# Performance work log

Measured on AMD Instinct MI355X. Metric: run time of the kernel, lower is better.

The kernel has to match this reference:

```python
import jax, jax.numpy as jnp
import numpy as np

N_NODES = 50000


def _gcn_conv(x, W, b, src, dst, n_nodes):
    """PyG-style GCNConv: add self-loops, symmetric normalization,
    transform-then-propagate: out = D^-1/2 A_hat D^-1/2 (x W) + b."""
    # add self loops
    loop = jnp.arange(n_nodes, dtype=src.dtype)
    s = jnp.concatenate([src, loop])
    d = jnp.concatenate([dst, loop])
    # degree (edge weight = 1) computed on destination nodes, incl. self loops
    deg = jax.ops.segment_sum(jnp.ones_like(d, dtype=x.dtype), d, num_segments=n_nodes)
    dinv = jnp.where(deg > 0, jax.lax.rsqrt(deg), 0.0)
    norm = dinv[s] * dinv[d]                      # [E+N]
    h = x @ W                                      # [N, F_out]
    msg = h[s] * norm[:, None]                     # [E+N, F_out] gather
    out = jax.ops.segment_sum(msg, d, num_segments=n_nodes)  # scatter-add
    return out + b


def setup_inputs() -> dict:
    key = jax.random.key(0)
    ks = jax.random.split(key, 12)
    N, E = N_NODES, 800000
    input_dim, hidden_dim, latent_dim, output_dim = 256, 64, 32, 3

    def glorot(k, fan_in, fan_out):
        lim = float(np.sqrt(6.0 / (fan_in + fan_out)))
        return jax.random.uniform(k, (fan_in, fan_out), jnp.float32, -lim, lim)

    return {
        "x": jax.random.normal(ks[0], (N, input_dim), jnp.float32),
        "edge_index": jax.random.randint(ks[1], (2, E), 0, N, jnp.int64 if jax.config.jax_enable_x64 else jnp.int32),
        "edge_attr": jax.random.normal(ks[2], (E,), jnp.float32),
        "W_enc_gnn": glorot(ks[3], input_dim, hidden_dim),
        "b_enc_gnn": jnp.zeros((hidden_dim,), jnp.float32),
        "W_enc_fc": glorot(ks[4], hidden_dim, latent_dim),
        "b_enc_fc": jnp.zeros((latent_dim,), jnp.float32),
        "W_dec_fc": glorot(ks[5], latent_dim, hidden_dim),
        "b_dec_fc": jnp.zeros((hidden_dim,), jnp.float32),
        "W_dec_gnn": glorot(ks[6], hidden_dim, input_dim),
        "b_dec_gnn": jnp.zeros((input_dim,), jnp.float32),
        "W_cond": glorot(ks[7], latent_dim, output_dim),
        "b_cond": jnp.zeros((output_dim,), jnp.float32),
    }


def reference(x, edge_index, edge_attr,
              W_enc_gnn, b_enc_gnn, W_enc_fc, b_enc_fc,
              W_dec_fc, b_dec_fc, W_dec_gnn, b_dec_gnn,
              W_cond, b_cond):
    n = x.shape[0]
    src, dst = edge_index[0], edge_index[1]
    # encode
    h = jax.nn.relu(_gcn_conv(x, W_enc_gnn, b_enc_gnn, src, dst, n))
    z = h @ W_enc_fc + b_enc_fc
    # decode
    hd = jax.nn.relu(z @ W_dec_fc + b_dec_fc)
    x_recon = _gcn_conv(hd, W_dec_gnn, b_dec_gnn, src, dst, n)
    # condition head
    pred = z @ W_cond + b_cond
    return (x_recon, z, pred)
```

## Files before the change

### kernel.cpp

```cpp
#include <hip/hip_runtime.h>
#include <stdint.h>

typedef _Float16 f16;
typedef _Float16 half4 __attribute__((ext_vector_type(4)));
typedef _Float16 f16x8 __attribute__((ext_vector_type(8)));
typedef float f32x4 __attribute__((ext_vector_type(4)));


#define BKT_SH 8
#define BKT_SZ 256
#define EB 4096
#define BCAP 16384

struct __attribute__((aligned(16))) G1S { f16 WB[4 * 8 * 64 * 8]; f16 Ah[64 * 136]; };
struct BinS { int h[256], segs[256], cur[256]; };
struct CsrS { int cnt[256], exc[256], cur2[256], p[256]; };
union __attribute__((aligned(16))) SmemU { G1S g1; BinS bin; CsrS csr; };


__device__ __forceinline__ void dev_binA2(SmemU& sm, const int* __restrict__ src,
                                          const int* __restrict__ dst, int E,
                                          int* __restrict__ bcur, unsigned* __restrict__ ebuf,
                                          int bid) {
    int* h = sm.bin.h; int* segs = sm.bin.segs; int* cur = sm.bin.cur;
    int tid = threadIdx.x;
    h[tid] = 0; cur[tid] = 0;
    __syncthreads();
    int base = bid * EB;
    int end = min(base + EB, E);
    for (int i = base + tid; i < end; i += 256) atomicAdd(&h[dst[i] >> BKT_SH], 1);
    __syncthreads();
    segs[tid] = h[tid] ? atomicAdd(&bcur[tid], h[tid]) : 0;
    __syncthreads();
    for (int i = base + tid; i < end; i += 256) {
        int d = dst[i];
        int bk = d >> BKT_SH;
        int r = atomicAdd(&cur[bk], 1);
        ebuf[(size_t)bk * BCAP + segs[bk] + r] =
            (unsigned)src[i] | ((unsigned)(d & (BKT_SZ - 1)) << 17);
    }
}

__device__ __forceinline__ void dev_csr2(SmemU& sm, const unsigned* __restrict__ ebuf,
                                         const int* __restrict__ bcur, int n, int E,
                                         int* __restrict__ row_ptr, float* __restrict__ dinv,
                                         int* __restrict__ ssorted, int b) {
    int* cnt = sm.csr.cnt; int* exc = sm.csr.exc; int* cur2 = sm.csr.cur2; int* p = sm.csr.p;
    int tid = threadIdx.x;
    int v = bcur[tid];
    p[tid] = v;
    __syncthreads();
    for (int o = 1; o < 256; o <<= 1) {
        int t = (tid >= o) ? p[tid - o] : 0;
        __syncthreads();
        p[tid] += t;
        __syncthreads();
    }
    int scnt = bcur[b];
    int s0 = p[b] - scnt;
    __syncthreads();
    if (b == 0 && tid == 0) row_ptr[n] = E;

    const unsigned* eb = &ebuf[(size_t)b * BCAP];
    int d0 = b << BKT_SH;
    int ndl = min(BKT_SZ, n - d0);
    cnt[tid] = 0; cur2[tid] = 0;
    __syncthreads();
    for (int i = tid; i < scnt; i += 256)
        atomicAdd(&cnt[(eb[i] >> 17) & (BKT_SZ - 1)], 1);
    __syncthreads();
    int c = cnt[tid];
    p[tid] = c;
    __syncthreads();
    for (int o = 1; o < 256; o <<= 1) {
        int t = (tid >= o) ? p[tid - o] : 0;
        __syncthreads();
        p[tid] += t;
        __syncthreads();
    }
    int exc_t = p[tid] - c;
    exc[tid] = exc_t;
    if (tid < ndl) {
        row_ptr[d0 + tid] = s0 + exc_t;
        dinv[d0 + tid] = rsqrtf((float)(c + 1));
    }
    __syncthreads();
    for (int i = tid; i < scnt; i += 256) {
        unsigned e = eb[i];
        int dl = (e >> 17) & (BKT_SZ - 1);
        int r = atomicAdd(&cur2[dl], 1);
        ssorted[s0 + exc[dl] + r] = (int)(e & 0x1FFFF);
    }
}

__device__ __forceinline__ void dev_gemm1(SmemU& sm, const float* __restrict__ x,
                                          const float* __restrict__ W, f16* __restrict__ out,
                                          int n, int tile) {
    f16* WB = sm.g1.WB;
    f16* Ah = sm.g1.Ah;
    int tid = threadIdx.x;
    int row0 = tile * 64;

    for (int i = tid; i < 4096; i += 256) {
        int k = i >> 4, c4 = (i & 15) * 4;
        float4 w = *(const float4*)&W[k * 64 + c4];
        int t = c4 >> 4, ks = k >> 5, q = (k & 31) >> 3, j = k & 7;
        int base = (((t * 8 + ks) * 64 + q * 16 + (c4 & 15)) * 8) + j;
        WB[base + 0]  = (f16)w.x;
        WB[base + 8]  = (f16)w.y;
        WB[base + 16] = (f16)w.z;
        WB[base + 24] = (f16)w.w;
    }

    int lane = tid & 63, w = tid >> 6;
    int m = lane & 15, q = lane >> 4;

    f32x4 acc[4];
#pragma unroll
    for (int t = 0; t < 4; t++) acc[t] = (f32x4){0.f, 0.f, 0.f, 0.f};

    for (int h = 0; h < 2; h++) {
        __syncthreads();
        for (int i = tid; i < 2048; i += 256) {
            int r = i >> 5, k4 = (i & 31) * 4;
            float4 v = {0.f, 0.f, 0.f, 0.f};
            if (row0 + r < n) v = *(const float4*)&x[(size_t)(row0 + r) * 256 + 128 * h + k4];
            half4 hv;
            hv.x = (f16)v.x; hv.y = (f16)v.y; hv.z = (f16)v.z; hv.w = (f16)v.w;
            *(half4*)&Ah[r * 136 + k4] = hv;
        }
        __syncthreads();
#pragma unroll
        for (int ksl = 0; ksl < 4; ksl++) {
            int ks = 4 * h + ksl;
            f16x8 a = *(const f16x8*)&Ah[(16 * w + m) * 136 + 32 * ksl + 8 * q];
#pragma unroll
            for (int t = 0; t < 4; t++) {
                f16x8 b = *(const f16x8*)&WB[((t * 8 + ks) * 64 + lane) * 8];
                acc[t] = __builtin_amdgcn_mfma_f32_16x16x32_f16(a, b, acc[t], 0, 0, 0);
            }
        }
    }

#pragma unroll
    for (int t = 0; t < 4; t++) {
#pragma unroll
        for (int r = 0; r < 4; r++) {
            int gr = row0 + 16 * w + 4 * q + r;
            if (gr < n) out[(size_t)gr * 64 + 16 * t + m] = (f16)acc[t][r];
        }
    }
}


__global__ __launch_bounds__(256) void k_p1(const int* __restrict__ src, const int* __restrict__ dst,
                                            int E, int* __restrict__ bcur, unsigned* __restrict__ ebuf,
                                            const float* __restrict__ x, const float* __restrict__ W,
                                            f16* __restrict__ out, int n, int nA, int tile0) {
    __shared__ SmemU sm;
    if ((int)blockIdx.x < nA) dev_binA2(sm, src, dst, E, bcur, ebuf, blockIdx.x);
    else dev_gemm1(sm, x, W, out, n, tile0 + (int)blockIdx.x - nA);
}

__global__ __launch_bounds__(256) void k_p2(const unsigned* __restrict__ ebuf,
                                            const int* __restrict__ bcur, int n, int E,
                                            int* __restrict__ row_ptr, float* __restrict__ dinv,
                                            int* __restrict__ ssorted,
                                            const float* __restrict__ x, const float* __restrict__ W,
                                            f16* __restrict__ out, int nA, int tile0) {
    __shared__ SmemU sm;
    if ((int)blockIdx.x < nA) dev_csr2(sm, ebuf, bcur, n, E, row_ptr, dinv, ssorted, blockIdx.x);
    else dev_gemm1(sm, x, W, out, n, tile0 + (int)blockIdx.x - nA);
}


#define GCN_GATHER(hpre, d, fg, AX, AY, AZ, AW, DD)                                     \
    {                                                                                   \
        half4 hs_ = *(const half4*)&hpre[(size_t)(d) * 64 + 4 * (fg)];                  \
        AX = DD * (float)hs_.x; AY = DD * (float)hs_.y;                                 \
        AZ = DD * (float)hs_.z; AW = DD * (float)hs_.w;                                 \
        int s0_ = row_ptr[d], s1_ = row_ptr[(d) + 1];                                   \
        for (int base_ = s0_; base_ < s1_; base_ += 16) {                               \
            int j_ = base_ + (fg);                                                      \
            int slv_ = 0;                                                               \
            float wl_ = 0.f;                                                            \
            if (j_ < s1_) { slv_ = ssorted[j_]; wl_ = dinv[slv_]; }                     \
            int cnt_ = min(16, s1_ - base_);                                            \
            for (int i_ = 0; i_ < cnt_; i_ += 8) {                                      \
                int a0 = __shfl(slv_, i_ + 0, 16), a1 = __shfl(slv_, i_ + 1, 16);       \
                int a2 = __shfl(slv_, i_ + 2, 16), a3 = __shfl(slv_, i_ + 3, 16);       \
                int a4 = __shfl(slv_, i_ + 4, 16), a5 = __shfl(slv_, i_ + 5, 16);       \
                int a6 = __shfl(slv_, i_ + 6, 16), a7 = __shfl(slv_, i_ + 7, 16);       \
                float w0 = __shfl(wl_, i_ + 0, 16), w1 = __shfl(wl_, i_ + 1, 16);       \
                float w2 = __shfl(wl_, i_ + 2, 16), w3 = __shfl(wl_, i_ + 3, 16);       \
                float w4 = __shfl(wl_, i_ + 4, 16), w5 = __shfl(wl_, i_ + 5, 16);       \
                float w6 = __shfl(wl_, i_ + 6, 16), w7 = __shfl(wl_, i_ + 7, 16);       \
                half4 h0 = *(const half4*)&hpre[(size_t)a0 * 64 + 4 * (fg)];            \
                half4 h1 = *(const half4*)&hpre[(size_t)a1 * 64 + 4 * (fg)];            \
                half4 h2 = *(const half4*)&hpre[(size_t)a2 * 64 + 4 * (fg)];            \
                half4 h3 = *(const half4*)&hpre[(size_t)a3 * 64 + 4 * (fg)];            \
                half4 h4 = *(const half4*)&hpre[(size_t)a4 * 64 + 4 * (fg)];            \
                half4 h5 = *(const half4*)&hpre[(size_t)a5 * 64 + 4 * (fg)];            \
                half4 h6 = *(const half4*)&hpre[(size_t)a6 * 64 + 4 * (fg)];            \
                half4 h7 = *(const half4*)&hpre[(size_t)a7 * 64 + 4 * (fg)];            \
                AX += w0 * (float)h0.x; AY += w0 * (float)h0.y;                         \
                AZ += w0 * (float)h0.z; AW += w0 * (float)h0.w;                         \
                AX += w1 * (float)h1.x; AY += w1 * (float)h1.y;                         \
                AZ += w1 * (float)h1.z; AW += w1 * (float)h1.w;                         \
                AX += w2 * (float)h2.x; AY += w2 * (float)h2.y;                         \
                AZ += w2 * (float)h2.z; AW += w2 * (float)h2.w;                         \
                AX += w3 * (float)h3.x; AY += w3 * (float)h3.y;                         \
                AZ += w3 * (float)h3.z; AW += w3 * (float)h3.w;                         \
                AX += w4 * (float)h4.x; AY += w4 * (float)h4.y;                         \
                AZ += w4 * (float)h4.z; AW += w4 * (float)h4.w;                         \
                AX += w5 * (float)h5.x; AY += w5 * (float)h5.y;                         \
                AZ += w5 * (float)h5.z; AW += w5 * (float)h5.w;                         \
                AX += w6 * (float)h6.x; AY += w6 * (float)h6.y;                         \
                AZ += w6 * (float)h6.z; AW += w6 * (float)h6.w;                         \
                AX += w7 * (float)h7.x; AY += w7 * (float)h7.y;                         \
                AZ += w7 * (float)h7.z; AW += w7 * (float)h7.w;                         \
            }                                                                           \
        }                                                                               \
    }


__global__ __launch_bounds__(256, 4) void k_midf(const f16* __restrict__ h1pre,
                                                 const int* __restrict__ row_ptr,
                                                 const int* __restrict__ ssorted,
                                                 const float* __restrict__ dinv,
                                                 const float* __restrict__ benc,
                                                 const float* __restrict__ Wz, const float* __restrict__ bz,
                                                 const float* __restrict__ Wd, const float* __restrict__ bd,
                                                 const float* __restrict__ Wc, const float* __restrict__ bc,
                                                 f16* __restrict__ hd_ws,
                                                 float* __restrict__ z_out, float* __restrict__ pred_out,
                                                 int n) {
    __shared__ __attribute__((aligned(16))) f16 Ah[64 * 72];
    __shared__ __attribute__((aligned(16))) f16 Zh[64 * 40];
    __shared__ __attribute__((aligned(16))) f16 WzB[2 * 2 * 64 * 8];
    __shared__ __attribute__((aligned(16))) f16 WdB[4 * 64 * 8];
    __shared__ float Wcs[32 * 4];
    __shared__ float bzs[32], bds[64], bcs[4], bes[64];
    int tid = threadIdx.x;
    int row0 = blockIdx.x * 64;

    for (int i = tid; i < 2048; i += 256) {
        int k = i >> 5, c = i & 31;
        int ks = k >> 5, q = (k >> 3) & 3, j = k & 7;
        int t = c >> 4, ln = q * 16 + (c & 15);
        WzB[((t * 2 + ks) * 64 + ln) * 8 + j] = (f16)Wz[i];
    }
    for (int i = tid; i < 2048; i += 256) {
        int k = i >> 6, c = i & 63;
        int q = k >> 3, j = k & 7;
        int t = c >> 4, ln = q * 16 + (c & 15);
        WdB[(t * 64 + ln) * 8 + j] = (f16)Wd[i];
    }
    if (tid < 96) Wcs[(tid / 3) * 4 + (tid % 3)] = Wc[tid];
    if (tid < 32) bzs[tid] = bz[tid];
    if (tid < 64) bds[tid] = bd[tid];
    if (tid < 3)  bcs[tid] = bc[tid];
    if (tid < 64) bes[tid] = benc[tid];
    __syncthreads();

    int lane = tid & 63, wid = tid >> 6;
    int g = lane >> 4, fg = lane & 15;

    for (int r = 0; r < 4; r++) {
        int no = 16 * wid + 4 * r + g;
        int d = row0 + no;
        float vx = 0.f, vy = 0.f, vz = 0.f, vw = 0.f;
        if (d < n) {
            float dd = dinv[d];
            float ax, ay, az, aw;
            GCN_GATHER(h1pre, d, fg, ax, ay, az, aw, dd);
            float4 b = *(float4*)&bes[4 * fg];
            vx = fmaxf(dd * ax + b.x, 0.f); vy = fmaxf(dd * ay + b.y, 0.f);
            vz = fmaxf(dd * az + b.z, 0.f); vw = fmaxf(dd * aw + b.w, 0.f);
        }
        half4 hv;
        hv.x = (f16)vx; hv.y = (f16)vy; hv.z = (f16)vz; hv.w = (f16)vw;
        *(half4*)&Ah[no * 72 + 4 * fg] = hv;
    }
    __syncthreads();

    int m = lane & 15, q = lane >> 4;

    f32x4 za[2];
    za[0] = (f32x4){0.f, 0.f, 0.f, 0.f};
    za[1] = (f32x4){0.f, 0.f, 0.f, 0.f};
#pragma unroll
    for (int ks = 0; ks < 2; ks++) {
        f16x8 a = *(const f16x8*)&Ah[(16 * wid + m) * 72 + 32 * ks + 8 * q];
#pragma unroll
        for (int t = 0; t < 2; t++) {
            f16x8 b = *(const f16x8*)&WzB[((t * 2 + ks) * 64 + lane) * 8];
            za[t] = __builtin_amdgcn_mfma_f32_16x16x32_f16(a, b, za[t], 0, 0, 0);
        }
    }
#pragma unroll
    for (int t = 0; t < 2; t++) {
        float bj = bzs[16 * t + m];
#pragma unroll
        for (int r = 0; r < 4; r++) {
            int node = 16 * wid + 4 * q + r;
            float zv = za[t][r] + bj;
            Zh[node * 40 + 16 * t + m] = (f16)zv;
            if (row0 + node < n) z_out[(size_t)(row0 + node) * 32 + 16 * t + m] = zv;
        }
    }
    __syncthreads();

    f16x8 a2 = *(const f16x8*)&Zh[(16 * wid + m) * 40 + 8 * q];
    f32x4 hb[4];
#pragma unroll
    for (int t = 0; t < 4; t++) {
        f16x8 b = *(const f16x8*)&WdB[(t * 64 + lane) * 8];
        f32x4 zero = (f32x4){0.f, 0.f, 0.f, 0.f};
        hb[t] = __builtin_amdgcn_mfma_f32_16x16x32_f16(a2, b, zero, 0, 0, 0);
    }
#pragma unroll
    for (int t = 0; t < 4; t++) {
        float bf = bds[16 * t + m];
#pragma unroll
        for (int r = 0; r < 4; r++) {
            int node = 16 * wid + 4 * q + r;
            if (row0 + node < n)
                hd_ws[(size_t)(row0 + node) * 64 + 16 * t + m] = (f16)fmaxf(hb[t][r] + bf, 0.f);
        }
    }

    if (tid < 64) {
        int node = tid;
        float pa = bcs[0], pb = bcs[1], pc = bcs[2];
        for (int k = 0; k < 32; k++) {
            float zv = (float)Zh[node * 40 + k];
            pa += zv * Wcs[k * 4 + 0];
            pb += zv * Wcs[k * 4 + 1];
            pc += zv * Wcs[k * 4 + 2];
        }
        if (row0 + node < n) {
            pred_out[(size_t)(row0 + node) * 3 + 0] = pa;
            pred_out[(size_t)(row0 + node) * 3 + 1] = pb;
            pred_out[(size_t)(row0 + node) * 3 + 2] = pc;
        }
    }
}


__global__ __launch_bounds__(256, 4) void k_decf(const f16* __restrict__ hd,
                                                 const int* __restrict__ row_ptr,
                                                 const int* __restrict__ ssorted,
                                                 const float* __restrict__ dinv,
                                                 const float* __restrict__ W,
                                                 const float* __restrict__ bias,
                                                 float* __restrict__ out, int n) {
    __shared__ __attribute__((aligned(16))) f16 WBh[8 * 2 * 64 * 8];
    __shared__ __attribute__((aligned(16))) f16 Ah[64 * 72];
    __shared__ float bs[256];
    int tid = threadIdx.x;
    int row0 = blockIdx.x * 64;

    bs[tid] = bias[tid];

    int lane = tid & 63, wid = tid >> 6;
    int g = lane >> 4, fg = lane & 15;

    for (int r = 0; r < 4; r++) {
        int no = 16 * wid + 4 * r + g;
        int d = row0 + no;
        float vx = 0.f, vy = 0.f, vz = 0.f, vw = 0.f;
        if (d < n) {
            float dd = dinv[d];
            float ax, ay, az, aw;
            GCN_GATHER(hd, d, fg, ax, ay, az, aw, dd);
            vx = dd * ax; vy = dd * ay; vz = dd * az; vw = dd * aw;
        }
        half4 hv;
        hv.x = (f16)vx; hv.y = (f16)vy; hv.z = (f16)vz; hv.w = (f16)vw;
        *(half4*)&Ah[no * 72 + 4 * fg] = hv;
    }
    __syncthreads();

    int m = lane & 15, q = lane >> 4;

    f16x8 a0 = *(const f16x8*)&Ah[(16 * wid + m) * 72 + 0 + 8 * q];
    f16x8 a1 = *(const f16x8*)&Ah[(16 * wid + m) * 72 + 32 + 8 * q];

    int gr0 = row0 + 16 * wid + 4 * q;
    bool full = (gr0 + 3 < n);

    for (int hf = 0; hf < 2; hf++) {
        __syncthreads();
        for (int i = tid; i < 2048; i += 256) {
            int k = i >> 5;
            int c4 = (i & 31) * 4 + 128 * hf;
            float4 w4 = *(const float4*)&W[k * 256 + c4];
            int ks = k >> 5, q2 = (k >> 3) & 3, j = k & 7;
            int tl = (c4 >> 4) - 8 * hf;
            int basei = ((tl * 2 + ks) * 64 + q2 * 16 + (c4 & 15)) * 8 + j;
            WBh[basei + 0]  = (f16)w4.x;
            WBh[basei + 8]  = (f16)w4.y;
            WBh[basei + 16] = (f16)w4.z;
            WBh[basei + 24] = (f16)w4.w;
        }
        __syncthreads();
#pragma unroll
        for (int tl = 0; tl < 8; tl++) {
            int t = 8 * hf + tl;
            f32x4 acc = (f32x4){0.f, 0.f, 0.f, 0.f};
            f16x8 b0 = *(const f16x8*)&WBh[((tl * 2 + 0) * 64 + lane) * 8];
            acc = __builtin_amdgcn_mfma_f32_16x16x32_f16(a0, b0, acc, 0, 0, 0);
            f16x8 b1 = *(const f16x8*)&WBh[((tl * 2 + 1) * 64 + lane) * 8];
            acc = __builtin_amdgcn_mfma_f32_16x16x32_f16(a1, b1, acc, 0, 0, 0);
            float bf = bs[16 * t + m];
            if (full) {
#pragma unroll
                for (int r = 0; r < 4; r++)
                    out[(size_t)(gr0 + r) * 256 + 16 * t + m] = acc[r] + bf;
            } else {
#pragma unroll
                for (int r = 0; r < 4; r++)
                    if (gr0 + r < n) out[(size_t)(gr0 + r) * 256 + 16 * t + m] = acc[r] + bf;
            }
        }
    }
}


extern "C" void kernel_launch(void* const* d_in, const int* in_sizes, int n_in,
                              void* d_out, int out_size, void* d_ws, size_t ws_size,
                              hipStream_t stream) {
    const float* x    = (const float*)d_in[0];
    const int*   ei   = (const int*)d_in[1];
    const float* Wenc = (const float*)d_in[3];
    const float* benc = (const float*)d_in[4];
    const float* Wz   = (const float*)d_in[5];
    const float* bz   = (const float*)d_in[6];
    const float* Wd   = (const float*)d_in[7];
    const float* bd   = (const float*)d_in[8];
    const float* Wdec = (const float*)d_in[9];
    const float* bdec = (const float*)d_in[10];
    const float* Wc   = (const float*)d_in[11];
    const float* bc   = (const float*)d_in[12];

    int n = in_sizes[0] / 256;
    int E = in_sizes[1] / 2;
    const int* src = ei;
    const int* dst = ei + E;

    int nbk = (n + BKT_SZ - 1) >> BKT_SH;
    int nbin = (E + EB - 1) / EB;

    char* w = (char*)d_ws;
    size_t off = 0;
    auto alloc = [&](size_t bytes) {
        void* p = w + off;
        off = (off + bytes + 255) & ~(size_t)255;
        return p;
    };
    int*      row_ptr = (int*)alloc(sizeof(int) * (n + 1));
    int*      ssorted = (int*)alloc(sizeof(int) * E);
    unsigned* ebuf    = (unsigned*)alloc(sizeof(unsigned) * (size_t)nbk * BCAP);
    float*    dinv    = (float*)alloc(sizeof(float) * n);
    int*      bcur    = (int*)alloc(sizeof(int) * 256);
    f16*      bufA    = (f16*)alloc(sizeof(f16) * (size_t)n * 64);
    f16*      bufB    = (f16*)alloc(sizeof(f16) * (size_t)n * 64);
    (void)ws_size; (void)n_in; (void)out_size;

    float* out_xr = (float*)d_out;
    float* out_z  = out_xr + (size_t)n * 256;
    float* out_p  = out_z + (size_t)n * 32;

    int tiles = (n + 63) / 64;
    int th = tiles / 2;

    hipMemsetAsync(bcur, 0, sizeof(int) * 256, stream);

    k_p1<<<dim3(nbin + th), dim3(256), 0, stream>>>(src, dst, E, bcur, ebuf,
                                                    x, Wenc, bufA, n, nbin, 0);
    k_p2<<<dim3(nbk + (tiles - th)), dim3(256), 0, stream>>>(ebuf, bcur, n, E, row_ptr, dinv, ssorted,
                                                             x, Wenc, bufA, nbk, th);

    k_midf<<<dim3(tiles), dim3(256), 0, stream>>>(bufA, row_ptr, ssorted, dinv, benc,
                                                  Wz, bz, Wd, bd, Wc, bc,
                                                  bufB, out_z, out_p, n);

    k_decf<<<dim3(tiles), dim3(256), 0, stream>>>(bufB, row_ptr, ssorted, dinv,
                                                  Wdec, bdec, out_xr, n);
}
```

Measured before the change: 226.8 us.

## Double block size for mid/decoder kernels and restage weights as packed f16x8 writes

Launches k_midf and k_decf with 512 threads (8 waves) per 64-node tile, halving the per-wave gather work and splitting the MFMA output columns across two wave groups. The decoder weight matrix is now staged into shared memory once, in full, instead of in two halves separated by barriers. Weight staging in all GEMM paths now builds each f16x8 fragment per thread with strided global reads and a single vector LDS store, replacing scattered scalar LDS stores. This trades more LDS per decoder block and uncoalesced weight loads for better latency hiding and fewer barriers.

```diff
diff --git a/kernel.cpp b/kernel.cpp
--- a/kernel.cpp
+++ b/kernel.cpp
@@ -101,15 +101,14 @@
     int tid = threadIdx.x;
     int row0 = tile * 64;
 
-    for (int i = tid; i < 4096; i += 256) {
-        int k = i >> 4, c4 = (i & 15) * 4;
-        float4 w = *(const float4*)&W[k * 64 + c4];
-        int t = c4 >> 4, ks = k >> 5, q = (k & 31) >> 3, j = k & 7;
-        int base = (((t * 8 + ks) * 64 + q * 16 + (c4 & 15)) * 8) + j;
-        WB[base + 0]  = (f16)w.x;
-        WB[base + 8]  = (f16)w.y;
-        WB[base + 16] = (f16)w.z;
-        WB[base + 24] = (f16)w.w;
+    for (int i = tid; i < 2048; i += 256) {
+        int m = i & 15, q = (i >> 4) & 3, ks = (i >> 6) & 7, t = i >> 9;
+        int col = 16 * t + m;
+        int k0 = ks * 32 + q * 8;
+        f16x8 v;
+#pragma unroll
+        for (int j = 0; j < 8; j++) v[j] = (f16)W[(k0 + j) * 64 + col];
+        *(f16x8*)&WB[i * 8] = v;
     }
 
     int lane = tid & 63, w = tid >> 6;
@@ -224,7 +223,7 @@
     }
 
 
-__global__ __launch_bounds__(256, 4) void k_midf(const f16* __restrict__ h1pre,
+__global__ __launch_bounds__(512, 6) void k_midf(const f16* __restrict__ h1pre,
                                                  const int* __restrict__ row_ptr,
                                                  const int* __restrict__ ssorted,
                                                  const float* __restrict__ dinv,
@@ -244,17 +243,24 @@
     int tid = threadIdx.x;
     int row0 = blockIdx.x * 64;
 
-    for (int i = tid; i < 2048; i += 256) {
-        int k = i >> 5, c = i & 31;
-        int ks = k >> 5, q = (k >> 3) & 3, j = k & 7;
-        int t = c >> 4, ln = q * 16 + (c & 15);
-        WzB[((t * 2 + ks) * 64 + ln) * 8 + j] = (f16)Wz[i];
-    }
-    for (int i = tid; i < 2048; i += 256) {
-        int k = i >> 6, c = i & 63;
-        int q = k >> 3, j = k & 7;
-        int t = c >> 4, ln = q * 16 + (c & 15);
-        WdB[(t * 64 + ln) * 8 + j] = (f16)Wd[i];
+    if (tid < 256) {
+        int i = tid;
+        int m = i & 15, q = (i >> 4) & 3, ks = (i >> 6) & 1, t = i >> 7;
+        int col = 16 * t + m;
+        int k0 = ks * 32 + q * 8;
+        f16x8 v;
+#pragma unroll
+        for (int j = 0; j < 8; j++) v[j] = (f16)Wz[(k0 + j) * 32 + col];
+        *(f16x8*)&WzB[i * 8] = v;
+    } else {
+        int i = tid - 256;
+        int m = i & 15, q = (i >> 4) & 3, t = i >> 6;
+        int col = 16 * t + m;
+        int k0 = q * 8;
+        f16x8 v;
+#pragma unroll
+        for (int j = 0; j < 8; j++) v[j] = (f16)Wd[(k0 + j) * 64 + col];
+        *(f16x8*)&WdB[i * 8] = v;
     }
     if (tid < 96) Wcs[(tid / 3) * 4 + (tid % 3)] = Wc[tid];
     if (tid < 32) bzs[tid] = bz[tid];
@@ -266,8 +272,8 @@
     int lane = tid & 63, wid = tid >> 6;
     int g = lane >> 4, fg = lane & 15;
 
-    for (int r = 0; r < 4; r++) {
-        int no = 16 * wid + 4 * r + g;
+    for (int r = 0; r < 2; r++) {
+        int no = 32 * r + 4 * wid + g;
         int d = row0 + no;
         float vx = 0.f, vy = 0.f, vz = 0.f, vw = 0.f;
         if (d < n) {
@@ -285,48 +291,40 @@
     __syncthreads();
 
     int m = lane & 15, q = lane >> 4;
-
-    f32x4 za[2];
-    za[0] = (f32x4){0.f, 0.f, 0.f, 0.f};
-    za[1] = (f32x4){0.f, 0.f, 0.f, 0.f};
+    int rowg = wid & 3, tsel = wid >> 2;
+
+    f32x4 za = (f32x4){0.f, 0.f, 0.f, 0.f};
 #pragma unroll
     for (int ks = 0; ks < 2; ks++) {
-        f16x8 a = *(const f16x8*)&Ah[(16 * wid + m) * 72 + 32 * ks + 8 * q];
-#pragma unroll
-        for (int t = 0; t < 2; t++) {
-            f16x8 b = *(const f16x8*)&WzB[((t * 2 + ks) * 64 + lane) * 8];
-            za[t] = __builtin_amdgcn_mfma_f32_16x16x32_f16(a, b, za[t], 0, 0, 0);
-        }
-    }
-#pragma unroll
-    for (int t = 0; t < 2; t++) {
-        float bj = bzs[16 * t + m];
+        f16x8 a = *(const f16x8*)&Ah[(16 * rowg + m) * 72 + 32 * ks + 8 * q];
+        f16x8 b = *(const f16x8*)&WzB[((tsel * 2 + ks) * 64 + lane) * 8];
+        za = __builtin_amdgcn_mfma_f32_16x16x32_f16(a, b, za, 0, 0, 0);
+    }
+    {
+        float bj = bzs[16 * tsel + m];
 #pragma unroll
         for (int r = 0; r < 4; r++) {
-            int node = 16 * wid + 4 * q + r;
-            float zv = za[t][r] + bj;
-            Zh[node * 40 + 16 * t + m] = (f16)zv;
-            if (row0 + node < n) z_out[(size_t)(row0 + node) * 32 + 16 * t + m] = zv;
-        }
-    }
-    __syncthreads();
-
-    f16x8 a2 = *(const f16x8*)&Zh[(16 * wid + m) * 40 + 8 * q];
-    f32x4 hb[4];
-#pragma unroll
-    for (int t = 0; t < 4; t++) {
+            int node = 16 * rowg + 4 * q + r;
+            float zv = za[r] + bj;
+            Zh[node * 40 + 16 * tsel + m] = (f16)zv;
+            if (row0 + node < n) z_out[(size_t)(row0 + node) * 32 + 16 * tsel + m] = zv;
+        }
+    }
+    __syncthreads();
+
+    f16x8 a2 = *(const f16x8*)&Zh[(16 * rowg + m) * 40 + 8 * q];
+#pragma unroll
+    for (int tt = 0; tt < 2; tt++) {
+        int t = 2 * tsel + tt;
+        f32x4 zero = (f32x4){0.f, 0.f, 0.f, 0.f};
         f16x8 b = *(const f16x8*)&WdB[(t * 64 + lane) * 8];
-        f32x4 zero = (f32x4){0.f, 0.f, 0.f, 0.f};
-        hb[t] = __builtin_amdgcn_mfma_f32_16x16x32_f16(a2, b, zero, 0, 0, 0);
-    }
-#pragma unroll
-    for (int t = 0; t < 4; t++) {
+        f32x4 hb = __builtin_amdgcn_mfma_f32_16x16x32_f16(a2, b, zero, 0, 0, 0);
         float bf = bds[16 * t + m];
 #pragma unroll
         for (int r = 0; r < 4; r++) {
-            int node = 16 * wid + 4 * q + r;
+            int node = 16 * rowg + 4 * q + r;
             if (row0 + node < n)
-                hd_ws[(size_t)(row0 + node) * 64 + 16 * t + m] = (f16)fmaxf(hb[t][r] + bf, 0.f);
+                hd_ws[(size_t)(row0 + node) * 64 + 16 * t + m] = (f16)fmaxf(hb[r] + bf, 0.f);
         }
     }
 
@@ -348,26 +346,36 @@
 }
 
 
-__global__ __launch_bounds__(256, 4) void k_decf(const f16* __restrict__ hd,
+__global__ __launch_bounds__(512, 6) void k_decf(const f16* __restrict__ hd,
                                                  const int* __restrict__ row_ptr,
                                                  const int* __restrict__ ssorted,
                                                  const float* __restrict__ dinv,
                                                  const float* __restrict__ W,
                                                  const float* __restrict__ bias,
                                                  float* __restrict__ out, int n) {
-    __shared__ __attribute__((aligned(16))) f16 WBh[8 * 2 * 64 * 8];
+    __shared__ __attribute__((aligned(16))) f16 WB[16 * 2 * 64 * 8];
     __shared__ __attribute__((aligned(16))) f16 Ah[64 * 72];
     __shared__ float bs[256];
     int tid = threadIdx.x;
     int row0 = blockIdx.x * 64;
 
-    bs[tid] = bias[tid];
+    if (tid < 256) bs[tid] = bias[tid];
+
+    for (int i = tid; i < 2048; i += 512) {
+        int m = i & 15, q = (i >> 4) & 3, ks = (i >> 6) & 1, t = i >> 7;
+        int col = 16 * t + m;
+        int k0 = ks * 32 + q * 8;
+        f16x8 v;
+#pragma unroll
+        for (int j = 0; j < 8; j++) v[j] = (f16)W[(k0 + j) * 256 + col];
+        *(f16x8*)&WB[i * 8] = v;
+    }
 
     int lane = tid & 63, wid = tid >> 6;
     int g = lane >> 4, fg = lane & 15;
 
-    for (int r = 0; r < 4; r++) {
-        int no = 16 * wid + 4 * r + g;
+    for (int r = 0; r < 2; r++) {
+        int no = 32 * r + 4 * wid + g;
         int d = row0 + no;
         float vx = 0.f, vy = 0.f, vz = 0.f, vw = 0.f;
         if (d < n) {
@@ -383,46 +391,30 @@
     __syncthreads();
 
     int m = lane & 15, q = lane >> 4;
-
-    f16x8 a0 = *(const f16x8*)&Ah[(16 * wid + m) * 72 + 0 + 8 * q];
-    f16x8 a1 = *(const f16x8*)&Ah[(16 * wid + m) * 72 + 32 + 8 * q];
-
-    int gr0 = row0 + 16 * wid + 4 * q;
+    int rowg = wid & 3, th = wid >> 2;
+
+    f16x8 a0 = *(const f16x8*)&Ah[(16 * rowg + m) * 72 + 0 + 8 * q];
+    f16x8 a1 = *(const f16x8*)&Ah[(16 * rowg + m) * 72 + 32 + 8 * q];
+
+    int gr0 = row0 + 16 * rowg + 4 * q;
     bool full = (gr0 + 3 < n);
-
-    for (int hf = 0; hf < 2; hf++) {
-        __syncthreads();
-        for (int i = tid; i < 2048; i += 256) {
-            int k = i >> 5;
-            int c4 = (i & 31) * 4 + 128 * hf;
-            float4 w4 = *(const float4*)&W[k * 256 + c4];
-            int ks = k >> 5, q2 = (k >> 3) & 3, j = k & 7;
-            int tl = (c4 >> 4) - 8 * hf;
-            int basei = ((tl * 2 + ks) * 64 + q2 * 16 + (c4 & 15)) * 8 + j;
-            WBh[basei + 0]  = (f16)w4.x;
-            WBh[basei + 8]  = (f16)w4.y;
-            WBh[basei + 16] = (f16)w4.z;
-            WBh[basei + 24] = (f16)w4.w;
-        }
-        __syncthreads();
-#pragma unroll
-        for (int tl = 0; tl < 8; tl++) {
-            int t = 8 * hf + tl;
-            f32x4 acc = (f32x4){0.f, 0.f, 0.f, 0.f};
-            f16x8 b0 = *(const f16x8*)&WBh[((tl * 2 + 0) * 64 + lane) * 8];
-            acc = __builtin_amdgcn_mfma_f32_16x16x32_f16(a0, b0, acc, 0, 0, 0);
-            f16x8 b1 = *(const f16x8*)&WBh[((tl * 2 + 1) * 64 + lane) * 8];
-            acc = __builtin_amdgcn_mfma_f32_16x16x32_f16(a1, b1, acc, 0, 0, 0);
-            float bf = bs[16 * t + m];
-            if (full) {
-#pragma unroll
-                for (int r = 0; r < 4; r++)
-                    out[(size_t)(gr0 + r) * 256 + 16 * t + m] = acc[r] + bf;
-            } else {
-#pragma unroll
-                for (int r = 0; r < 4; r++)
-                    if (gr0 + r < n) out[(size_t)(gr0 + r) * 256 + 16 * t + m] = acc[r] + bf;
-            }
+#pragma unroll 4
+    for (int tl = 0; tl < 8; tl++) {
+        int t = 8 * th + tl;
+        f32x4 acc = (f32x4){0.f, 0.f, 0.f, 0.f};
+        f16x8 b0 = *(const f16x8*)&WB[((t * 2 + 0) * 64 + lane) * 8];
+        acc = __builtin_amdgcn_mfma_f32_16x16x32_f16(a0, b0, acc, 0, 0, 0);
+        f16x8 b1 = *(const f16x8*)&WB[((t * 2 + 1) * 64 + lane) * 8];
+        acc = __builtin_amdgcn_mfma_f32_16x16x32_f16(a1, b1, acc, 0, 0, 0);
+        float bf = bs[16 * t + m];
+        if (full) {
+#pragma unroll
+            for (int r = 0; r < 4; r++)
+                out[(size_t)(gr0 + r) * 256 + 16 * t + m] = acc[r] + bf;
+        } else {
+#pragma unroll
+            for (int r = 0; r < 4; r++)
+                if (gr0 + r < n) out[(size_t)(gr0 + r) * 256 + 16 * t + m] = acc[r] + bf;
         }
     }
 }
@@ -482,10 +474,10 @@
     k_p2<<<dim3(nbk + (tiles - th)), dim3(256), 0, stream>>>(ebuf, bcur, n, E, row_ptr, dinv, ssorted,
                                                              x, Wenc, bufA, nbk, th);
 
-    k_midf<<<dim3(tiles), dim3(256), 0, stream>>>(bufA, row_ptr, ssorted, dinv, benc,
+    k_midf<<<dim3(tiles), dim3(512), 0, stream>>>(bufA, row_ptr, ssorted, dinv, benc,
                                                   Wz, bz, Wd, bd, Wc, bc,
                                                   bufB, out_z, out_p, n);
 
-    k_decf<<<dim3(tiles), dim3(256), 0, stream>>>(bufB, row_ptr, ssorted, dinv,
+    k_decf<<<dim3(tiles), dim3(512), 0, stream>>>(bufB, row_ptr, ssorted, dinv,
                                                   Wdec, bdec, out_xr, n);
 }
```

New measurement: 212.9 us. 6.2% less time.
